# Performance work log

Hardware: AMD Instinct MI355X
Metric: run time of the kernel (lower is better)

The kernel has to match this reference:

```python
import jax, jax.numpy as jnp
import numpy as np

# Grid constants from point_cloud_range and PILLAR_SIZE (KITTI PointPillars defaults)
PX, PY, PZ = 0.16, 0.16, 4.0
X0, Y0, Z0 = 0.0, -39.68, -3.0
NX, NY, NZ = 432, 496, 1
X_OFF = PX / 2 + X0
Y_OFF = PY / 2 + Y0
Z_OFF = PZ / 2 + Z0
B = 8          # batch size
P = 96000      # total pillars across batch
M = 32         # max points per pillar
CIN = 10       # 4 base + 3 cluster + 3 center
COUT = 64      # FILTERS[-1]
BN_EPS = 1e-3


def setup_inputs() -> dict:
    key = jax.random.key(0)
    k1, k2, k3, k4, k5, k6 = jax.random.split(key, 6)
    pillars = jax.random.normal(k1, (P, M, 4), dtype=jnp.float32)
    b = jax.random.randint(k2, (P,), 0, B, dtype=jnp.int32)
    z = jnp.zeros((P,), dtype=jnp.int32)  # nz == 1
    y = jax.random.randint(k3, (P,), 0, NY, dtype=jnp.int32)
    x = jax.random.randint(k4, (P,), 0, NX, dtype=jnp.int32)
    coords = jnp.stack([b, z, y, x], axis=1)  # (P, 4) as [batch, z, y, x]
    num_points = jax.random.randint(k5, (P,), 1, M + 1, dtype=jnp.int32)
    W = jax.random.normal(k6, (CIN, COUT), dtype=jnp.float32) * 0.05
    gamma = jnp.ones((COUT,), dtype=jnp.float32)
    beta = jnp.zeros((COUT,), dtype=jnp.float32)
    return {"pillars": pillars, "coords": coords, "num_points": num_points,
            "W": W, "gamma": gamma, "beta": beta}


def _pfe_forward(pillars, W, gamma, beta, coords, num_points):
    # --- feature augmentation ---
    abs_xyz = pillars[:, :, :3]                                   # (P, M, 3)
    n = num_points.astype(pillars.dtype)[:, None, None]
    mean_xyz = jnp.sum(abs_xyz, axis=1, keepdims=True) / n        # (P, 1, 3)
    xyz_to_cluster = abs_xyz - mean_xyz                           # (P, M, 3)
    cz = coords[:, 1].astype(pillars.dtype)
    cy = coords[:, 2].astype(pillars.dtype)
    cx = coords[:, 3].astype(pillars.dtype)
    centers = jnp.stack([cx * PX + X_OFF, cy * PY + Y_OFF, cz * PZ + Z_OFF], axis=-1)
    xyz_to_center = abs_xyz - centers[:, None, :]                 # (P, M, 3)
    feats = jnp.concatenate([pillars, xyz_to_cluster, xyz_to_center], axis=-1)  # (P, M, 10)

    # --- PFNLayer: linear (no bias) + BatchNorm1d (train-mode batch stats) + ReLU + max over points ---
    h = jnp.einsum("pmi,io->pmo", feats, W)                       # (P, M, COUT)
    mu = jnp.mean(h, axis=(0, 1))
    var = jnp.var(h, axis=(0, 1))                                 # biased, like torch BN
    h = (h - mu) * jax.lax.rsqrt(var + BN_EPS) * gamma + beta
    h = jax.nn.relu(h)
    pv = jnp.max(h, axis=1)                                       # (P, COUT)

    # --- scatter pillar features to dense BEV grid ---
    cell = coords[:, 1] + coords[:, 2] * NX + coords[:, 3]        # z + y*nx + x
    flat = coords[:, 0] * (NZ * NY * NX) + cell                   # (P,)
    bev = jnp.zeros((B * NZ * NY * NX, COUT), dtype=pv.dtype).at[flat].set(pv)
    bev = bev.reshape(B, NZ * NY * NX, COUT).transpose(0, 2, 1)   # (B, C, nz*ny*nx)
    return bev.reshape(B, COUT * NZ, NY, NX)


def reference(pillars, coords, num_points, W, gamma, beta):
    return _pfe_forward(pillars, W, gamma, beta, coords, num_points)
```

## Files before the change

kernel.cpp:

```cpp
#include <hip/hip_runtime.h>

#define NPILLARS 96000
#define MPTS 32
#define NCHAN 64
#define NXC 432
#define NYC 496
#define NB 8
#define NCELLS (NXC*NYC)
#define NBLK 1024
#define PXc 0.16f
#define PYc 0.16f
#define PZc 4.0f
#define XOFF (0.08f)
#define YOFF (0.08f - 39.68f)
#define ZOFF (2.0f - 3.0f)
#define BN_EPS 1e-3f

typedef __attribute__((ext_vector_type(8))) short short8;
typedef __attribute__((ext_vector_type(16))) float float16;
typedef __attribute__((ext_vector_type(4))) float natf4;

__device__ __forceinline__ int f2bf(float x) {
    union { float f; unsigned u; } v; v.f = x;
    unsigned r = v.u + 0x7FFFu + ((v.u >> 16) & 1u);
    return (int)(r >> 16);
}

#define PAIRS(Q) \
 Q(0,0,0) Q(1,0,1) Q(2,0,2) Q(3,0,3) Q(4,0,4) Q(5,0,5) Q(6,0,6) Q(7,0,7) Q(8,0,8) Q(9,0,9) \
 Q(10,1,1) Q(11,1,2) Q(12,1,3) Q(13,1,4) Q(14,1,5) Q(15,1,6) Q(16,1,7) Q(17,1,8) Q(18,1,9) \
 Q(19,2,2) Q(20,2,3) Q(21,2,4) Q(22,2,5) Q(23,2,6) Q(24,2,7) Q(25,2,8) Q(26,2,9) \
 Q(27,3,3) Q(28,3,4) Q(29,3,5) Q(30,3,6) Q(31,3,7) Q(32,3,8) Q(33,3,9) \
 Q(34,4,4) Q(35,4,5) Q(36,4,6) Q(37,4,7) Q(38,4,8) Q(39,4,9) \
 Q(40,5,5) Q(41,5,6) Q(42,5,7) Q(43,5,8) Q(44,5,9) \
 Q(45,6,6) Q(46,6,7) Q(47,6,8) Q(48,6,9) \
 Q(49,7,7) Q(50,7,8) Q(51,7,9) \
 Q(52,8,8) Q(53,8,9) \
 Q(54,9,9)

__global__ __launch_bounds__(256, 3)
void k_fused(const float4* __restrict__ pillars,
             const int4* __restrict__ coords,
             const int* __restrict__ num_points,
             const float* __restrict__ W,
             float* __restrict__ pvmax,
             float* __restrict__ mom,
             int* __restrict__ winner) {
    const int tid  = threadIdx.x;
    const int lane = tid & 63;
    const int sub  = lane & 31;
    const int half = lane >> 5;
    const int wv   = tid >> 6;
    const int wid    = (blockIdx.x * blockDim.x + tid) >> 6;
    const int nwaves = (gridDim.x * blockDim.x) >> 6;

    short8 bf0, bf1;
#pragma unroll
    for (int r = 0; r < 8; r++) {
        const int k = half * 8 + r;
        bf0[r] = (k < 10) ? (short)f2bf(W[k * NCHAN + sub])      : (short)0;
        bf1[r] = (k < 10) ? (short)f2bf(W[k * NCHAN + 32 + sub]) : (short)0;
    }

    float s0=0.f,s1=0.f,s2=0.f,s3=0.f,s4=0.f,s5=0.f,s6=0.f,s7=0.f,s8=0.f,s9=0.f;
#define QDECL(idx,i,j) float q_##i##_##j = 0.f;
    PAIRS(QDECL)
#undef QDECL

    for (int base = wid * 2; base < NPILLARS; base += nwaves * 2) {
        const int p = base + half;
        float4 pt = pillars[p * MPTS + sub];
        float sx = pt.x, sy = pt.y, sz = pt.z;
#pragma unroll
        for (int m = 16; m >= 1; m >>= 1) {
            sx += __shfl_xor(sx, m);
            sy += __shfl_xor(sy, m);
            sz += __shfl_xor(sz, m);
        }
        const float n = (float)num_points[p];
        const float mx = sx / n, my = sy / n, mz = sz / n;
        const int4  cd = coords[p];
        const float ctx = (float)cd.w * PXc + XOFF;
        const float cty = (float)cd.z * PYc + YOFF;
        const float ctz = (float)cd.y * PZc + ZOFF;
        const float f0=pt.x, f1=pt.y, f2=pt.z, f3=pt.w;
        const float f4=pt.x-mx,  f5=pt.y-my,  f6=pt.z-mz;
        const float f7=pt.x-ctx, f8=pt.y-cty, f9=pt.z-ctz;
        s0+=f0; s1+=f1; s2+=f2; s3+=f3; s4+=f4;
        s5+=f5; s6+=f6; s7+=f7; s8+=f8; s9+=f9;
#define QACC(idx,i,j) q_##i##_##j = fmaf(f##i, f##j, q_##i##_##j);
        PAIRS(QACC)
#undef QACC
        const int b0 = f2bf(f0), b1 = f2bf(f1), b2 = f2bf(f2), b3 = f2bf(f3),
                  b4 = f2bf(f4), b5 = f2bf(f5), b6 = f2bf(f6), b7 = f2bf(f7),
                  b8 = f2bf(f8), b9 = f2bf(f9);
        const int s8b = __shfl(b8, sub),      s9b = __shfl(b9, sub);
        const int t0 = __shfl(b0, sub + 32), t1 = __shfl(b1, sub + 32),
                  t2 = __shfl(b2, sub + 32), t3 = __shfl(b3, sub + 32),
                  t4 = __shfl(b4, sub + 32), t5 = __shfl(b5, sub + 32),
                  t6 = __shfl(b6, sub + 32), t7 = __shfl(b7, sub + 32);
        short8 a0v;
        a0v[0] = (short)(half ? s8b : b0);
        a0v[1] = (short)(half ? s9b : b1);
        a0v[2] = half ? (short)0 : (short)b2;
        a0v[3] = half ? (short)0 : (short)b3;
        a0v[4] = half ? (short)0 : (short)b4;
        a0v[5] = half ? (short)0 : (short)b5;
        a0v[6] = half ? (short)0 : (short)b6;
        a0v[7] = half ? (short)0 : (short)b7;
        short8 a1v;
        a1v[0] = (short)(half ? b8 : t0);
        a1v[1] = (short)(half ? b9 : t1);
        a1v[2] = half ? (short)0 : (short)t2;
        a1v[3] = half ? (short)0 : (short)t3;
        a1v[4] = half ? (short)0 : (short)t4;
        a1v[5] = half ? (short)0 : (short)t5;
        a1v[6] = half ? (short)0 : (short)t6;
        a1v[7] = half ? (short)0 : (short)t7;
        float16 accA0 = {}, accA1 = {}, accB0 = {}, accB1 = {};
        accA0 = __builtin_amdgcn_mfma_f32_32x32x16_bf16(a0v, bf0, accA0, 0, 0, 0);
        accA1 = __builtin_amdgcn_mfma_f32_32x32x16_bf16(a0v, bf1, accA1, 0, 0, 0);
        accB0 = __builtin_amdgcn_mfma_f32_32x32x16_bf16(a1v, bf0, accB0, 0, 0, 0);
        accB1 = __builtin_amdgcn_mfma_f32_32x32x16_bf16(a1v, bf1, accB1, 0, 0, 0);
        float mA0 = -3.4e38f, mA1 = -3.4e38f, mB0 = -3.4e38f, mB1 = -3.4e38f;
#pragma unroll
        for (int r = 0; r < 16; r++) {
            mA0 = fmaxf(mA0, accA0[r]);  mA1 = fmaxf(mA1, accA1[r]);
            mB0 = fmaxf(mB0, accB0[r]);  mB1 = fmaxf(mB1, accB1[r]);
        }
        mA0 = fmaxf(mA0, __shfl_xor(mA0, 32));  mA1 = fmaxf(mA1, __shfl_xor(mA1, 32));
        mB0 = fmaxf(mB0, __shfl_xor(mB0, 32));  mB1 = fmaxf(mB1, __shfl_xor(mB1, 32));
        pvmax[base * NCHAN + lane]       = half ? mA1 : mA0;
        pvmax[(base + 1) * NCHAN + lane] = half ? mB1 : mB0;
        if (sub == 0) {
            const int cell = cd.y + cd.z * NXC + cd.w;
            atomicMax(&winner[cd.x * NCELLS + cell], p + 1);
        }
    }

    __shared__ float lds_part[4][65];
#define RED6(v) { v += __shfl_xor(v,32); v += __shfl_xor(v,16); v += __shfl_xor(v,8); \
                  v += __shfl_xor(v,4);  v += __shfl_xor(v,2);  v += __shfl_xor(v,1); }
    RED6(s0) RED6(s1) RED6(s2) RED6(s3) RED6(s4)
    RED6(s5) RED6(s6) RED6(s7) RED6(s8) RED6(s9)
#define QRED(idx,i,j) RED6(q_##i##_##j)
    PAIRS(QRED)
#undef QRED
#undef RED6
    if (lane == 0) {
        float* dst = &lds_part[wv][0];
        dst[0]=s0; dst[1]=s1; dst[2]=s2; dst[3]=s3; dst[4]=s4;
        dst[5]=s5; dst[6]=s6; dst[7]=s7; dst[8]=s8; dst[9]=s9;
#define QST(idx,i,j) dst[10+idx] = q_##i##_##j;
        PAIRS(QST)
#undef QST
    }
    __syncthreads();
    if (tid < 65) {
        const float acc = lds_part[0][tid] + lds_part[1][tid]
                        + lds_part[2][tid] + lds_part[3][tid];
        atomicAdd(&mom[tid], acc);
    }
}

__global__ void k_expand(const int* __restrict__ winner,
                         const float* __restrict__ pvmax,
                         const float* __restrict__ mom,
                         const float* __restrict__ W,
                         const float* __restrict__ gamma,
                         const float* __restrict__ beta,
                         float* __restrict__ out) {
    __shared__ float s_sc[64], s_sh[64];
    const int t = threadIdx.x;
    if (t < 64) {
        const float invN = 1.0f / ((float)NPILLARS * (float)MPTS);
        float wv0=W[0*NCHAN+t], wv1=W[1*NCHAN+t], wv2=W[2*NCHAN+t], wv3=W[3*NCHAN+t],
              wv4=W[4*NCHAN+t], wv5=W[5*NCHAN+t], wv6=W[6*NCHAN+t], wv7=W[7*NCHAN+t],
              wv8=W[8*NCHAN+t], wv9=W[9*NCHAN+t];
        float mu = mom[0]*wv0 + mom[1]*wv1 + mom[2]*wv2 + mom[3]*wv3 + mom[4]*wv4
                 + mom[5]*wv5 + mom[6]*wv6 + mom[7]*wv7 + mom[8]*wv8 + mom[9]*wv9;
        mu *= invN;
        float e2 = 0.f;
#define QFOLD(idx,i,j) { float tt = mom[10+idx] * wv##i * wv##j; \
                         e2 += (i == j) ? tt : 2.0f * tt; }
        PAIRS(QFOLD)
#undef QFOLD
        e2 *= invN;
        const float var = e2 - mu * mu;
        const float scale = gamma[t] * rsqrtf(var + BN_EPS);
        const float shift = beta[t] - mu * scale;
        s_sc[t] = scale;
        s_sh[t] = shift;
    }
    __syncthreads();

    const int idx = blockIdx.x * blockDim.x + t;
    const int total4 = NB * NCELLS / 4;
    if (idx >= total4) return;
    const int b    = (idx << 2) / NCELLS;
    const int cell = (idx << 2) - b * NCELLS;
    const int4 w = ((const int4*)winner)[idx];
    const float mk0 = (w.x > 0) ? 1.f : 0.f;
    const float mk1 = (w.y > 0) ? 1.f : 0.f;
    const float mk2 = (w.z > 0) ? 1.f : 0.f;
    const float mk3 = (w.w > 0) ? 1.f : 0.f;
    const size_t r0 = (size_t)((w.x > 0) ? w.x - 1 : 0) * NCHAN;
    const size_t r1 = (size_t)((w.y > 0) ? w.y - 1 : 0) * NCHAN;
    const size_t r2 = (size_t)((w.z > 0) ? w.z - 1 : 0) * NCHAN;
    const size_t r3 = (size_t)((w.w > 0) ? w.w - 1 : 0) * NCHAN;
    float* obase = out + (size_t)b * NCHAN * NCELLS + cell;
#pragma unroll 2
    for (int g = 0; g < 16; g++) {
        natf4 a0 = *(const natf4*)(pvmax + r0 + 4*g);
        natf4 a1 = *(const natf4*)(pvmax + r1 + 4*g);
        natf4 a2 = *(const natf4*)(pvmax + r2 + 4*g);
        natf4 a3 = *(const natf4*)(pvmax + r3 + 4*g);
#pragma unroll
        for (int j = 0; j < 4; j++) {
            const int c = 4*g + j;
            const float sc = s_sc[c], sh = s_sh[c];
            natf4 v;
            v.x = mk0 * fmaxf(0.f, fmaf(a0[j], sc, sh));
            v.y = mk1 * fmaxf(0.f, fmaf(a1[j], sc, sh));
            v.z = mk2 * fmaxf(0.f, fmaf(a2[j], sc, sh));
            v.w = mk3 * fmaxf(0.f, fmaf(a3[j], sc, sh));
            *reinterpret_cast<natf4*>(obase + (size_t)c * NCELLS) = v;
        }
    }
}

extern "C" void kernel_launch(void* const* d_in, const int* in_sizes, int n_in,
                              void* d_out, int out_size, void* d_ws, size_t ws_size,
                              hipStream_t stream) {
    const float4* pillars    = (const float4*)d_in[0];
    const int4*   coords     = (const int4*)d_in[1];
    const int*    num_points = (const int*)d_in[2];
    const float*  W          = (const float*)d_in[3];
    const float*  gamma      = (const float*)d_in[4];
    const float*  beta       = (const float*)d_in[5];
    float* out = (float*)d_out;

    char* ws = (char*)d_ws;
    const size_t WIN_BYTES = (size_t)NB * NCELLS * sizeof(int);
    float* mom    = (float*)ws;
    int*   winner = (int*)(ws + 512);
    float* pvmax  = (float*)(ws + 512 + WIN_BYTES);

    (void)hipMemsetAsync(ws, 0, 512 + WIN_BYTES, stream);

    k_fused <<<NBLK, 256, 0, stream>>>(pillars, coords, num_points, W,
                                       pvmax, mom, winner);
    k_expand<<<(NB * NCELLS / 4) / 256, 256, 0, stream>>>(winner, pvmax,
                                                          mom, W, gamma, beta, out);
}
```

Measured before the change: 559.3 us.

## Split BN scale/shift into tiny kernel and map expand threads per channel-plane

The per-block BN scale/shift computation moves into a separate single-block kernel that writes to workspace, so the expand kernel no longer recomputes it in every block. The expand kernel now gives each thread four cells of a single channel plane rather than four cells across all 64 channels, which multiplies the thread count by 64 and makes each thread's work tiny. Output writes stay coalesced. Reads of pvmax become scalar gathers with a 256-byte stride, and the winner array is re-read once per channel, which may raise gather traffic. It also adds one more kernel launch.

```diff
diff --git a/kernel.cpp b/kernel.cpp
--- a/kernel.cpp
+++ b/kernel.cpp
@@ -7,6 +7,7 @@
 #define NYC 496
 #define NB 8
 #define NCELLS (NXC*NYC)
+#define PL4 (NCELLS/4)
 #define NBLK 1024
 #define PXc 0.16f
 #define PYc 0.16f
@@ -163,70 +164,55 @@
     }
 }
 
+__global__ void k_ss(const float* __restrict__ mom,
+                     const float* __restrict__ W,
+                     const float* __restrict__ gamma,
+                     const float* __restrict__ beta,
+                     float* __restrict__ ss) {
+    const int c = threadIdx.x;
+    const float invN = 1.0f / ((float)NPILLARS * (float)MPTS);
+    float wv0=W[0*NCHAN+c], wv1=W[1*NCHAN+c], wv2=W[2*NCHAN+c], wv3=W[3*NCHAN+c],
+          wv4=W[4*NCHAN+c], wv5=W[5*NCHAN+c], wv6=W[6*NCHAN+c], wv7=W[7*NCHAN+c],
+          wv8=W[8*NCHAN+c], wv9=W[9*NCHAN+c];
+    float mu = mom[0]*wv0 + mom[1]*wv1 + mom[2]*wv2 + mom[3]*wv3 + mom[4]*wv4
+             + mom[5]*wv5 + mom[6]*wv6 + mom[7]*wv7 + mom[8]*wv8 + mom[9]*wv9;
+    mu *= invN;
+    float e2 = 0.f;
+#define QFOLD(idx,i,j) { float tt = mom[10+idx] * wv##i * wv##j; \
+                         e2 += (i == j) ? tt : 2.0f * tt; }
+    PAIRS(QFOLD)
+#undef QFOLD
+    e2 *= invN;
+    const float var = e2 - mu * mu;
+    const float scale = gamma[c] * rsqrtf(var + BN_EPS);
+    ss[c] = scale;
+    ss[64 + c] = beta[c] - mu * scale;
+}
+
 __global__ void k_expand(const int* __restrict__ winner,
                          const float* __restrict__ pvmax,
-                         const float* __restrict__ mom,
-                         const float* __restrict__ W,
-                         const float* __restrict__ gamma,
-                         const float* __restrict__ beta,
+                         const float* __restrict__ ss,
                          float* __restrict__ out) {
-    __shared__ float s_sc[64], s_sh[64];
-    const int t = threadIdx.x;
-    if (t < 64) {
-        const float invN = 1.0f / ((float)NPILLARS * (float)MPTS);
-        float wv0=W[0*NCHAN+t], wv1=W[1*NCHAN+t], wv2=W[2*NCHAN+t], wv3=W[3*NCHAN+t],
-              wv4=W[4*NCHAN+t], wv5=W[5*NCHAN+t], wv6=W[6*NCHAN+t], wv7=W[7*NCHAN+t],
-              wv8=W[8*NCHAN+t], wv9=W[9*NCHAN+t];
-        float mu = mom[0]*wv0 + mom[1]*wv1 + mom[2]*wv2 + mom[3]*wv3 + mom[4]*wv4
-                 + mom[5]*wv5 + mom[6]*wv6 + mom[7]*wv7 + mom[8]*wv8 + mom[9]*wv9;
-        mu *= invN;
-        float e2 = 0.f;
-#define QFOLD(idx,i,j) { float tt = mom[10+idx] * wv##i * wv##j; \
-                         e2 += (i == j) ? tt : 2.0f * tt; }
-        PAIRS(QFOLD)
-#undef QFOLD
-        e2 *= invN;
-        const float var = e2 - mu * mu;
-        const float scale = gamma[t] * rsqrtf(var + BN_EPS);
-        const float shift = beta[t] - mu * scale;
-        s_sc[t] = scale;
-        s_sh[t] = shift;
-    }
-    __syncthreads();
-
-    const int idx = blockIdx.x * blockDim.x + t;
-    const int total4 = NB * NCELLS / 4;
-    if (idx >= total4) return;
-    const int b    = (idx << 2) / NCELLS;
-    const int cell = (idx << 2) - b * NCELLS;
-    const int4 w = ((const int4*)winner)[idx];
+    const int idx = blockIdx.x * blockDim.x + threadIdx.x;
+    const int plane = idx / PL4;
+    const int cg    = idx - plane * PL4;
+    const int b = plane >> 6, c = plane & 63;
+    const float sc = ss[c], sh = ss[64 + c];
+    const int4 w = ((const int4*)(winner + b * NCELLS))[cg];
     const float mk0 = (w.x > 0) ? 1.f : 0.f;
     const float mk1 = (w.y > 0) ? 1.f : 0.f;
     const float mk2 = (w.z > 0) ? 1.f : 0.f;
     const float mk3 = (w.w > 0) ? 1.f : 0.f;
-    const size_t r0 = (size_t)((w.x > 0) ? w.x - 1 : 0) * NCHAN;
-    const size_t r1 = (size_t)((w.y > 0) ? w.y - 1 : 0) * NCHAN;
-    const size_t r2 = (size_t)((w.z > 0) ? w.z - 1 : 0) * NCHAN;
-    const size_t r3 = (size_t)((w.w > 0) ? w.w - 1 : 0) * NCHAN;
-    float* obase = out + (size_t)b * NCHAN * NCELLS + cell;
-#pragma unroll 2
-    for (int g = 0; g < 16; g++) {
-        natf4 a0 = *(const natf4*)(pvmax + r0 + 4*g);
-        natf4 a1 = *(const natf4*)(pvmax + r1 + 4*g);
-        natf4 a2 = *(const natf4*)(pvmax + r2 + 4*g);
-        natf4 a3 = *(const natf4*)(pvmax + r3 + 4*g);
-#pragma unroll
-        for (int j = 0; j < 4; j++) {
-            const int c = 4*g + j;
-            const float sc = s_sc[c], sh = s_sh[c];
-            natf4 v;
-            v.x = mk0 * fmaxf(0.f, fmaf(a0[j], sc, sh));
-            v.y = mk1 * fmaxf(0.f, fmaf(a1[j], sc, sh));
-            v.z = mk2 * fmaxf(0.f, fmaf(a2[j], sc, sh));
-            v.w = mk3 * fmaxf(0.f, fmaf(a3[j], sc, sh));
-            *reinterpret_cast<natf4*>(obase + (size_t)c * NCELLS) = v;
-        }
-    }
+    const size_t r0 = (size_t)((w.x > 0) ? w.x - 1 : 0) * NCHAN + c;
+    const size_t r1 = (size_t)((w.y > 0) ? w.y - 1 : 0) * NCHAN + c;
+    const size_t r2 = (size_t)((w.z > 0) ? w.z - 1 : 0) * NCHAN + c;
+    const size_t r3 = (size_t)((w.w > 0) ? w.w - 1 : 0) * NCHAN + c;
+    natf4 v;
+    v.x = mk0 * fmaxf(0.f, fmaf(pvmax[r0], sc, sh));
+    v.y = mk1 * fmaxf(0.f, fmaf(pvmax[r1], sc, sh));
+    v.z = mk2 * fmaxf(0.f, fmaf(pvmax[r2], sc, sh));
+    v.w = mk3 * fmaxf(0.f, fmaf(pvmax[r3], sc, sh));
+    ((natf4*)out)[idx] = v;
 }
 
 extern "C" void kernel_launch(void* const* d_in, const int* in_sizes, int n_in,
@@ -243,13 +229,14 @@
     char* ws = (char*)d_ws;
     const size_t WIN_BYTES = (size_t)NB * NCELLS * sizeof(int);
     float* mom    = (float*)ws;
-    int*   winner = (int*)(ws + 512);
-    float* pvmax  = (float*)(ws + 512 + WIN_BYTES);
-
-    (void)hipMemsetAsync(ws, 0, 512 + WIN_BYTES, stream);
+    float* ss     = (float*)(ws + 256);
+    int*   winner = (int*)(ws + 1024);
+    float* pvmax  = (float*)(ws + 1024 + WIN_BYTES);
+
+    (void)hipMemsetAsync(ws, 0, 1024 + WIN_BYTES, stream);
 
     k_fused <<<NBLK, 256, 0, stream>>>(pillars, coords, num_points, W,
                                        pvmax, mom, winner);
-    k_expand<<<(NB * NCELLS / 4) / 256, 256, 0, stream>>>(winner, pvmax,
-                                                          mom, W, gamma, beta, out);
-}
+    k_ss    <<<1, 64, 0, stream>>>(mom, W, gamma, beta, ss);
+    k_expand<<<(NB * NCHAN * PL4) / 256, 256, 0, stream>>>(winner, pvmax, ss, out);
+}
```

Result: slower. 580.8 us (+3.9%).
